# Kernel optimization log

Hardware: AMD Instinct MI355X
Metric: run time of the kernel (lower is better)

The kernel has to match this reference:

```python
import jax, jax.numpy as jnp
import numpy as np

# Dims
B, C, D, H, W = 2, 64, 16, 64, 64
G = 2            # deformable groups (choose_group(64, 2) -> 2)
K = 27           # 3x3x3 kernel points
GC = C // G      # channels per group
AXIS = (0.5, 1.0, 1.0)   # offset_axis_scale (d, h, w)
EPS = 1e-5
# kernel point offsets for k=3, pad=1, dilation=1: {-1,0,1}^3
_KOFF = np.array([(a, b, c) for a in (-1, 0, 1) for b in (-1, 0, 1) for c in (-1, 0, 1)], dtype=np.float32)


def conv3d(x, w, b=None, pad=0):
    y = jax.lax.conv_general_dilated(x, w, (1, 1, 1), [(pad, pad)] * 3,
                                     dimension_numbers=('NCDHW', 'OIDHW', 'NCDHW'))
    if b is not None:
        y = y + b[None, :, None, None, None]
    return y


def proj1x1(x, w, b=None):
    y = jnp.einsum('oc,bcdhw->bodhw', w, x)
    if b is not None:
        y = y + b[None, :, None, None, None]
    return y


def _trilinear_sample(vflat, pd, ph, pw):
    # vflat: [B,G,GC,DHW]; pd/ph/pw: [B,G,DHW] float sampling coords; zeros padding outside
    d0 = jnp.floor(pd); h0 = jnp.floor(ph); w0 = jnp.floor(pw)
    td, th, tw = pd - d0, ph - h0, pw - w0
    d0 = d0.astype(jnp.int32); h0 = h0.astype(jnp.int32); w0 = w0.astype(jnp.int32)
    acc = jnp.zeros_like(vflat)
    for dd in (0, 1):
        for hh in (0, 1):
            for ww in (0, 1):
                di, hi, wi = d0 + dd, h0 + hh, w0 + ww
                valid = ((di >= 0) & (di < D) & (hi >= 0) & (hi < H) & (wi >= 0) & (wi < W)).astype(vflat.dtype)
                idx = (jnp.clip(di, 0, D - 1) * H + jnp.clip(hi, 0, H - 1)) * W + jnp.clip(wi, 0, W - 1)
                g = jnp.take_along_axis(vflat, jnp.broadcast_to(idx[:, :, None, :], vflat.shape), axis=3)
                wgt = ((td if dd else 1.0 - td) * (th if hh else 1.0 - th) * (tw if ww else 1.0 - tw)) * valid
                acc = acc + g * wgt[:, :, None, :]
    return acc


def setup_inputs() -> dict:
    key = jax.random.key(0)
    ks = jax.random.split(key, 8)
    f = jnp.float32
    s = 1.0 / np.sqrt(C)
    return {
        'x': jax.random.normal(ks[0], (B, C, D, H, W), f),
        'gate': jnp.zeros((), f),
        'pre_w': jax.random.normal(ks[1], (C, C, 1, 1, 1), f) * s,
        'post_w': jax.random.normal(ks[2], (C, C, 1, 1, 1), f) * s,
        'in_proj_w': jax.random.normal(ks[3], (C, C), f) * s,
        'in_proj_b': jnp.zeros((C,), f),
        'out_proj_w': jax.random.normal(ks[4], (C, C), f) * s,
        'out_proj_b': jnp.zeros((C,), f),
        'off_w': jax.random.normal(ks[5], (3 * G * K, C, 3, 3, 3), f) * 0.01,
        'off_b': jnp.zeros((3 * G * K,), f),
        'mask_w': jax.random.normal(ks[6], (G * K, C, 3, 3, 3), f) * 0.01,
        'mask_b': jnp.zeros((G * K,), f),
        'in_gamma': jnp.ones((C,), f),
        'in_beta': jnp.zeros((C,), f),
    }


def reference(x, gate, pre_w, post_w, in_proj_w, in_proj_b, out_proj_w, out_proj_b,
              off_w, off_b, mask_w, mask_b, in_gamma, in_beta):
    DHW = D * H * W
    xp = conv3d(x, pre_w)                                      # pre 1x1
    # --- DCNv3_3D: value projection, learned offsets + softmax modulation mask ---
    v = proj1x1(xp, in_proj_w, in_proj_b).reshape(B, G, GC, DHW)
    off = conv3d(xp, off_w, off_b, pad=1).reshape(B, G, K, 3, DHW)   # warmed-up offset_scale = 1.0
    m = jax.nn.softmax(conv3d(xp, mask_w, mask_b, pad=1).reshape(B, G, K, DHW), axis=2)
    dg, hg, wg = jnp.meshgrid(jnp.arange(D, dtype=jnp.float32),
                              jnp.arange(H, dtype=jnp.float32),
                              jnp.arange(W, dtype=jnp.float32), indexing='ij')
    dg, hg, wg = dg.reshape(-1), hg.reshape(-1), wg.reshape(-1)      # [DHW]
    out = jnp.zeros_like(v)
    for k in range(K):   # fixed small loop over 27 kernel points
        pd = dg + _KOFF[k, 0] + off[:, :, k, 0] * AXIS[0]
        ph = hg + _KOFF[k, 1] + off[:, :, k, 1] * AXIS[1]
        pw = wg + _KOFF[k, 2] + off[:, :, k, 2] * AXIS[2]
        out = out + _trilinear_sample(v, pd, ph, pw) * m[:, :, k, :][:, :, None, :]
    y = out.reshape(B, C, D, H, W)
    y = proj1x1(y, out_proj_w, out_proj_b)
    # InstanceNorm3d + GELU
    mu = y.mean(axis=(2, 3, 4), keepdims=True)
    var = y.var(axis=(2, 3, 4), keepdims=True)
    y = (y - mu) * jax.lax.rsqrt(var + EPS)
    y = y * in_gamma[None, :, None, None, None] + in_beta[None, :, None, None, None]
    y = jax.nn.gelu(y)
    y = conv3d(y, post_w)                                      # post 1x1
    return x + jax.nn.sigmoid(gate) * y
```

## Files before the change

### kernel.cpp

```cpp
#include <hip/hip_runtime.h>
#include <hip/hip_bf16.h>

typedef short short8 __attribute__((ext_vector_type(8)));
typedef float f32x4 __attribute__((ext_vector_type(4)));
typedef _Float16 h2 __attribute__((ext_vector_type(2)));
typedef _Float16 half8 __attribute__((ext_vector_type(8)));
typedef __fp16 fp16x2 __attribute__((ext_vector_type(2)));

#if __has_builtin(__builtin_elementwise_fma)
#define FMA2H(a, b, c) __builtin_elementwise_fma((a), (b), (c))
#else
#define FMA2H(a, b, c) ((a) * (b) + (c))
#endif

namespace {
constexpr int Bn = 2, Cn = 64, Dn = 16, Hn = 64, Wn = 64;
constexpr int Gn = 2, Kn = 27, GCn = 32;
constexpr int DHW = Dn * Hn * Wn;
constexpr int OCn = 216;
constexpr int PD = 18, PH = 66, PW = 66;
constexpr float EPS = 1e-5f;

constexpr int PROWS = 12 * 66;
constexpr int PATCH_B = PROWS * 128;

constexpr size_t XPADH_OFF = 0;
constexpr size_t XPADH_B   = (size_t)Bn * PD * PH * PW * Cn * 2;
constexpr size_t WFRAG_OFF = XPADH_OFF + XPADH_B;
constexpr size_t WFRAG_B   = (size_t)54 * 16 * 64 * 16;
constexpr size_t WV_OFF    = WFRAG_OFF + WFRAG_B;
constexpr size_t WV_B      = 64 * 64 * 4;
constexpr size_t CONV_OFF  = WV_OFF + WV_B;
constexpr size_t CONV_B    = (size_t)Bn * OCn * DHW * 2;
constexpr size_t V_OFF     = CONV_OFF + CONV_B;
constexpr size_t V_B       = (size_t)Bn * Gn * DHW * GCn * 2;
constexpr size_t SAMP_OFF  = V_OFF + V_B;
constexpr size_t SAMP_B    = (size_t)Bn * Gn * DHW * GCn * 2;
constexpr size_t STAT_OFF  = SAMP_OFF + SAMP_B;
constexpr size_t WVH_OFF   = STAT_OFF + 4096;
constexpr size_t WOH_OFF   = WVH_OFF + 8192;
constexpr size_t WPH_OFF   = WOH_OFF + 8192;
}

__device__ inline float b2f(short s) {
  union { float f; unsigned u; } x; x.u = ((unsigned)(unsigned short)s) << 16; return x.f;
}
__device__ inline short f2b(float f) {
  __hip_bfloat16 h = __float2bfloat16(f);
  union { __hip_bfloat16 h; short s; } x; x.h = h; return x.s;
}
__device__ inline int iclamp(int v, int lo, int hi) { return v < lo ? lo : (v > hi ? hi : v); }
__device__ inline h2 u2h2(unsigned u) {
  union { unsigned u; h2 h; } x; x.u = u; return x.h;
}
__device__ inline unsigned h2u(h2 h) {
  union { unsigned u; h2 h; } x; x.h = h; return x.u;
}
__device__ inline h2 pkrtz(float a, float b) {
#if __has_builtin(__builtin_amdgcn_cvt_pkrtz)
  union { fp16x2 p; h2 h; } x;
  x.p = __builtin_amdgcn_cvt_pkrtz(a, b);
  return x.h;
#else
  return (h2){(_Float16)a, (_Float16)b};
#endif
}

__global__ __launch_bounds__(256) void zerofill(uint4* __restrict__ p, int n16) {
  int i = blockIdx.x * 256 + threadIdx.x;
  if (i < n16) p[i] = make_uint4(0, 0, 0, 0);
}

__global__ __launch_bounds__(256) void fillpad(const float* __restrict__ x,
                                               __hip_bfloat16* __restrict__ xpadh) {
  int tid = threadIdx.x;
  int w5 = tid & 31, cq = tid >> 5;
  int p = blockIdx.x * 32 + w5;
  int b = blockIdx.y;
  int w = p & 63, h = (p >> 6) & 63, d = p >> 12;
  const float* xb = x + ((size_t)b * 64 + cq * 8) * DHW + p;
  short8 o8;
#pragma unroll
  for (int j = 0; j < 8; ++j) o8[j] = f2b(xb[(size_t)j * DHW]);
  __hip_bfloat16* ob = xpadh + (size_t)b * (PD * PH * PW * 64)
      + ((((size_t)(d + 1) * 66) + (h + 1)) * 66 + (w + 1)) * 64 + cq * 8;
  *(short8*)ob = o8;
}

__global__ __launch_bounds__(256) void fold_weights(
    const float* __restrict__ pre_w, const float* __restrict__ in_proj_w,
    const float* __restrict__ off_w, const float* __restrict__ mask_w,
    short8* __restrict__ Wfrag, float* __restrict__ Wv) {
  int i = blockIdx.x * 256 + threadIdx.x;
  if (i < 64 * 64) {
    int o = i >> 6, c = i & 63;
    float s = 0.f;
    for (int cp = 0; cp < 64; ++cp) s += in_proj_w[o * 64 + cp] * pre_w[cp * 64 + c];
    Wv[i] = s;
    return;
  }
  int t = i - 64 * 64;
  if (t >= 54 * 16 * 64) return;
  int l = t & 63; int rest = t >> 6;
  int mt = rest & 15; int ks = rest >> 4;
  int oc = mt * 16 + (l & 15);
  int tap = ks >> 1;
  int c0 = (ks & 1) * 32 + (l >> 4) * 8;
  float vals[8] = {0.f, 0.f, 0.f, 0.f, 0.f, 0.f, 0.f, 0.f};
  if (oc < OCn) {
    const float* cw = (oc < 162) ? (off_w + (size_t)oc * 64 * 27)
                                 : (mask_w + (size_t)(oc - 162) * 64 * 27);
#pragma unroll 1
    for (int cp = 0; cp < 64; ++cp) {
      float wv = cw[cp * 27 + tap];
      const float* pr = pre_w + cp * 64 + c0;
#pragma unroll
      for (int j = 0; j < 8; ++j) vals[j] += wv * pr[j];
    }
  }
  short8 o8;
#pragma unroll
  for (int j = 0; j < 8; ++j) o8[j] = f2b(vals[j]);
  Wfrag[t] = o8;
}

__global__ __launch_bounds__(256) void packw(
    const float* __restrict__ Wv, const float* __restrict__ Wout,
    const float* __restrict__ Wpost, h2* __restrict__ WvH,
    h2* __restrict__ WoutH, h2* __restrict__ WpostH) {
  int i = blockIdx.x * 256 + threadIdx.x;
  if (i < 2048) WvH[i] = pkrtz(Wv[2 * i], Wv[2 * i + 1]);
  else if (i < 4096) { int j = i - 2048; WoutH[j] = pkrtz(Wout[2 * j], Wout[2 * j + 1]); }
  else if (i < 6144) { int j = i - 4096; WpostH[j] = pkrtz(Wpost[2 * j], Wpost[2 * j + 1]); }
}

__global__ __launch_bounds__(256) void vproj(
    const float* __restrict__ x, const h2* __restrict__ WvH,
    const float* __restrict__ vb, _Float16* __restrict__ v) {
  int p = blockIdx.x * 256 + threadIdx.x;
  int b = blockIdx.y;
  const float* xb = x + (size_t)b * Cn * DHW;
  h2 xh[32];
#pragma unroll
  for (int j = 0; j < 32; ++j)
    xh[j] = pkrtz(xb[(2 * j) * DHW + p], xb[(2 * j + 1) * DHW + p]);
#pragma unroll 1
  for (int g = 0; g < Gn; ++g) {
    _Float16 vo[GCn];
#pragma unroll
    for (int jo = 0; jo < GCn; ++jo) {
      int o = g * GCn + jo;
      h2 a = (h2){(_Float16)0.f, (_Float16)0.f};
#pragma unroll
      for (int j = 0; j < 32; ++j) a = FMA2H(WvH[o * 32 + j], xh[j], a);
      vo[jo] = (_Float16)(vb[o] + (float)a[0] + (float)a[1]);
    }
    half8* dst = (half8*)(v + ((size_t)(b * Gn + g) * DHW + p) * GCn);
#pragma unroll
    for (int q = 0; q < 4; ++q) {
      half8 o8;
#pragma unroll
      for (int j = 0; j < 8; ++j) o8[j] = vo[q * 8 + j];
      dst[q] = o8;
    }
  }
}

__global__ __launch_bounds__(512) void conv_mfma(
    const char* __restrict__ xpadh, const char* __restrict__ wfrag,
    const float* __restrict__ off_b, const float* __restrict__ mask_b,
    __hip_bfloat16* __restrict__ convout) {
  __shared__ char lds[PATCH_B];
  int tid = threadIdx.x;
  int h0 = blockIdx.x * 2, d = blockIdx.y, b = blockIdx.z;

  const char* xb = xpadh + (size_t)b * (PD * PH * PW * 128);
  for (int idx = tid; idx < PROWS * 8; idx += 512) {
    int s = idx >> 3, slot = idx & 7;
    int r12 = s / 66, wx = s - r12 * 66;
    int dp = r12 >> 2, hp = r12 & 3;
    const char* g = xb + ((((size_t)(d + dp)) * 66 + (h0 + hp)) * 66 + wx) * 128 + slot * 16;
    *(uint4*)(lds + s * 128 + ((slot ^ (s & 7)) << 4)) = *(const uint4*)g;
  }
  __syncthreads();

  int wid = tid >> 6, l = tid & 63;
  int wm = wid & 3, wn = wid >> 2;
  int lm = l & 15, lk = l >> 4;
  const char* abase = wfrag + ((size_t)((wm * 4) * 64 + l)) * 16;

  f32x4 acc[4][4];
#pragma unroll
  for (int mt = 0; mt < 4; ++mt)
#pragma unroll
    for (int nt = 0; nt < 4; ++nt) acc[mt][nt] = (f32x4){0.f, 0.f, 0.f, 0.f};

  short8 A0[4], B0[4], A1[4], B1[4], A2[4], B2[4];

#define LOADA(KS, A)                                                          \
  {                                                                           \
    const char* ap_ = abase + (KS) * 16384;                                   \
    _Pragma("unroll")                                                         \
    for (int mt = 0; mt < 4; ++mt) A[mt] = *(const short8*)(ap_ + mt * 1024); \
  }
#define LOADB(KS, B)                                                          \
  {                                                                           \
    int tap_ = (KS) >> 1;                                                     \
    int dd_ = tap_ / 9, rem_ = tap_ - dd_ * 9;                                \
    int dh_ = rem_ / 3, dw_ = rem_ - dh_ * 3;                                 \
    int srow_ = (dd_ * 4 + wn + dh_) * 66 + dw_;                              \
    int uslot_ = 4 * ((KS) & 1) + lk;                                         \
    _Pragma("unroll")                                                         \
    for (int nt = 0; nt < 4; ++nt) {                                          \
      int sr_ = srow_ + nt * 16 + lm;                                         \
      B[nt] = *(const short8*)(lds + sr_ * 128 + ((uslot_ ^ (sr_ & 7)) << 4)); \
    }                                                                         \
  }
#define MFMAS(A, B)                                                           \
  __builtin_amdgcn_s_setprio(1);                                              \
  _Pragma("unroll")                                                           \
  for (int mt = 0; mt < 4; ++mt)                                              \
    _Pragma("unroll")                                                         \
    for (int nt = 0; nt < 4; ++nt)                                            \
      acc[mt][nt] = __builtin_amdgcn_mfma_f32_16x16x32_bf16(A[mt], B[nt], acc[mt][nt], 0, 0, 0); \
  __builtin_amdgcn_s_setprio(0);

  LOADA(0, A0) LOADB(0, B0)
  LOADA(1, A1) LOADB(1, B1)
#pragma unroll 1
  for (int ks = 0; ks < 54; ks += 3) {
    LOADA(ks + 2, A2) LOADB(ks + 2, B2)
    MFMAS(A0, B0)
    if (ks + 3 < 54) { LOADA(ks + 3, A0) LOADB(ks + 3, B0) }
    MFMAS(A1, B1)
    if (ks + 4 < 54) { LOADA(ks + 4, A1) LOADB(ks + 4, B1) }
    MFMAS(A2, B2)
  }
#undef LOADA
#undef LOADB
#undef MFMAS

  int pbase = d * 4096 + (h0 + wn) * 64;
#pragma unroll
  for (int mt = 0; mt < 4; ++mt) {
    int oc0 = wm * 64 + mt * 16 + lk * 4;
#pragma unroll
    for (int r = 0; r < 4; ++r) {
      int oc = oc0 + r;
      if (oc < OCn) {
        float bias = (oc < 162) ? off_b[oc] : mask_b[oc - 162];
        size_t orow = ((size_t)b * OCn + oc) * DHW + pbase;
#pragma unroll
        for (int nt = 0; nt < 4; ++nt)
          convout[orow + nt * 16 + lm] = __float2bfloat16(acc[mt][nt][r] + bias);
      }
    }
  }
}

__global__ __launch_bounds__(256) void dcn_sample(
    const __hip_bfloat16* __restrict__ convout, const _Float16* __restrict__ v,
    _Float16* __restrict__ sampled) {
  __shared__ short offm[108 * 64];
  int tid = threadIdx.x;
  int bg = blockIdx.y;
  int b = bg >> 1, g = bg & 1;
  int p0 = blockIdx.x * 64;

  const __hip_bfloat16* cb = convout + (size_t)b * OCn * DHW;
#pragma unroll 1
  for (int idx = tid; idx < 108 * 8; idx += 256) {
    int row = idx >> 3, col = idx & 7;
    int oc = (row < 81) ? (g * 81 + row) : (162 + g * Kn + (row - 81));
    *(uint4*)(offm + row * 64 + col * 8) = *(const uint4*)(cb + (size_t)oc * DHW + p0 + col * 8);
  }
  __syncthreads();

  int pl = tid >> 2, q = tid & 3;
  int p = p0 + pl;
  int w = p & 63, h = (p >> 6) & 63, d = p >> 12;

  float msum = 0.f;
  h2 acc[4];
#pragma unroll
  for (int j = 0; j < 4; ++j) acc[j] = (h2){(_Float16)0.f, (_Float16)0.f};
  const char* vg = (const char*)v + ((size_t)bg * DHW * GCn + q * 8) * 2;

#pragma unroll 1
  for (int k = 0; k < Kn; ++k) {
    float offd = b2f(offm[(3 * k + 0) * 64 + pl]);
    float offh = b2f(offm[(3 * k + 1) * 64 + pl]);
    float offw = b2f(offm[(3 * k + 2) * 64 + pl]);
    float pd = (float)(d + (k / 9) - 1) + offd * 0.5f;
    float ph = (float)(h + ((k / 3) % 3) - 1) + offh;
    float pw = (float)(w + (k % 3) - 1) + offw;
    float fd = floorf(pd), fh = floorf(ph), fw = floorf(pw);
    float td = pd - fd, th = ph - fh, tw = pw - fw;
    int d0 = (int)fd, h0 = (int)fh, w0 = (int)fw;
    float ek = __expf(b2f(offm[(81 + k) * 64 + pl]));
    msum += ek;

    float wd0 = ((unsigned)d0 < (unsigned)Dn) ? (1.f - td) * ek : 0.f;
    float wd1 = ((unsigned)(d0 + 1) < (unsigned)Dn) ? td * ek : 0.f;
    float wh0 = ((unsigned)h0 < (unsigned)Hn) ? (1.f - th) : 0.f;
    float wh1 = ((unsigned)(h0 + 1) < (unsigned)Hn) ? th : 0.f;
    float ww0 = ((unsigned)w0 < (unsigned)Wn) ? (1.f - tw) : 0.f;
    float ww1 = ((unsigned)(w0 + 1) < (unsigned)Wn) ? tw : 0.f;
    int dr0 = iclamp(d0, 0, Dn - 1) << 18, dr1 = iclamp(d0 + 1, 0, Dn - 1) << 18;
    int hr0 = iclamp(h0, 0, Hn - 1) << 12, hr1 = iclamp(h0 + 1, 0, Hn - 1) << 12;
    int wc0 = iclamp(w0, 0, Wn - 1) << 6,  wc1 = iclamp(w0 + 1, 0, Wn - 1) << 6;
    float wdh00 = wd0 * wh0, wdh01 = wd0 * wh1, wdh10 = wd1 * wh0, wdh11 = wd1 * wh1;

#define CORNER(BOFF, WT)                                                \
    {                                                                   \
      _Float16 wh_ = (_Float16)(WT);                                    \
      h2 w2_ = {wh_, wh_};                                              \
      uint4 u_ = *(const uint4*)(vg + (BOFF));                          \
      acc[0] = FMA2H(u2h2(u_.x), w2_, acc[0]);                          \
      acc[1] = FMA2H(u2h2(u_.y), w2_, acc[1]);                          \
      acc[2] = FMA2H(u2h2(u_.z), w2_, acc[2]);                          \
      acc[3] = FMA2H(u2h2(u_.w), w2_, acc[3]);                          \
    }
    CORNER(dr0 + hr0 + wc0, wdh00 * ww0)
    CORNER(dr0 + hr0 + wc1, wdh00 * ww1)
    CORNER(dr0 + hr1 + wc0, wdh01 * ww0)
    CORNER(dr0 + hr1 + wc1, wdh01 * ww1)
    CORNER(dr1 + hr0 + wc0, wdh10 * ww0)
    CORNER(dr1 + hr0 + wc1, wdh10 * ww1)
    CORNER(dr1 + hr1 + wc0, wdh11 * ww0)
    CORNER(dr1 + hr1 + wc1, wdh11 * ww1)
#undef CORNER
  }

  _Float16 rh = (_Float16)(1.f / msum);
  h2 rs2 = {rh, rh};
  uint4 ov;
  ov.x = h2u(acc[0] * rs2);
  ov.y = h2u(acc[1] * rs2);
  ov.z = h2u(acc[2] * rs2);
  ov.w = h2u(acc[3] * rs2);
  *(uint4*)((char*)sampled + ((size_t)bg * DHW + p) * 64 + q * 16) = ov;
}

__global__ __launch_bounds__(256) void outproj(
    const _Float16* __restrict__ sampled, const h2* __restrict__ WoutH,
    const float* __restrict__ ob, __hip_bfloat16* __restrict__ t) {
  int p = blockIdx.x * 256 + threadIdx.x;
  int b = blockIdx.y;
  h2 sv2[32];
#pragma unroll
  for (int g = 0; g < Gn; ++g) {
    const uint4* src = (const uint4*)(sampled + ((size_t)(b * Gn + g) * DHW + p) * GCn);
#pragma unroll
    for (int q = 0; q < 4; ++q) {
      uint4 uu = src[q];
      sv2[g * 16 + q * 4 + 0] = u2h2(uu.x);
      sv2[g * 16 + q * 4 + 1] = u2h2(uu.y);
      sv2[g * 16 + q * 4 + 2] = u2h2(uu.z);
      sv2[g * 16 + q * 4 + 3] = u2h2(uu.w);
    }
  }
#pragma unroll 1
  for (int o = 0; o < Cn; ++o) {
    h2 a = (h2){(_Float16)0.f, (_Float16)0.f};
#pragma unroll
    for (int j = 0; j < 32; ++j) a = FMA2H(WoutH[o * 32 + j], sv2[j], a);
    float s = ob[o] + (float)a[0] + (float)a[1];
    t[((size_t)b * Cn + o) * DHW + p] = __float2bfloat16(s);
  }
}

__global__ __launch_bounds__(256) void stats_k(const __hip_bfloat16* __restrict__ t,
                                               float* __restrict__ stat) {
  int bc = blockIdx.x;
  const short8* tc = (const short8*)(t + (size_t)bc * DHW);
  float s = 0.f, ss = 0.f;
  for (int i = threadIdx.x; i < DHW / 8; i += 256) {
    short8 s8 = tc[i];
#pragma unroll
    for (int j = 0; j < 8; ++j) { float xv = b2f(s8[j]); s += xv; ss += xv * xv; }
  }
#pragma unroll
  for (int o = 32; o > 0; o >>= 1) { s += __shfl_down(s, o); ss += __shfl_down(ss, o); }
  __shared__ float ls[4], lss[4];
  int wid = threadIdx.x >> 6;
  if ((threadIdx.x & 63) == 0) { ls[wid] = s; lss[wid] = ss; }
  __syncthreads();
  if (threadIdx.x == 0) {
    float S = ls[0] + ls[1] + ls[2] + ls[3];
    float SS = lss[0] + lss[1] + lss[2] + lss[3];
    float mu = S / (float)DHW;
    float var = SS / (float)DHW - mu * mu;
    stat[bc * 2 + 0] = mu;
    stat[bc * 2 + 1] = rsqrtf(var + EPS);
  }
}

__global__ __launch_bounds__(256) void finalk(
    const __hip_bfloat16* __restrict__ t, const float* __restrict__ x,
    const float* __restrict__ stat,
    const float* __restrict__ gamma, const float* __restrict__ beta,
    const h2* __restrict__ WpostH, const float* __restrict__ gate, float* out) {
  int p = blockIdx.x * 256 + threadIdx.x;
  int b = blockIdx.y;
  float sg = 1.f / (1.f + __expf(-gate[0]));
  float nv[Cn];
#pragma unroll
  for (int c = 0; c < Cn; ++c) {
    float mu = stat[(b * Cn + c) * 2 + 0];
    float rstd = stat[(b * Cn + c) * 2 + 1];
    float tv = b2f(((const short*)t)[((size_t)b * Cn + c) * DHW + p]);
    float yv = (tv - mu) * rstd * gamma[c] + beta[c];
    float u = 0.7978845608028654f * (yv + 0.044715f * yv * yv * yv);
    float e = __expf(2.f * u);
    float th = 1.f - 2.f / (e + 1.f);
    nv[c] = 0.5f * yv * (1.f + th);
  }
  h2 nh[32];
#pragma unroll
  for (int j = 0; j < 32; ++j) nh[j] = pkrtz(nv[2 * j], nv[2 * j + 1]);
#pragma unroll 1
  for (int o = 0; o < Cn; ++o) {
    h2 a = (h2){(_Float16)0.f, (_Float16)0.f};
#pragma unroll
    for (int j = 0; j < 32; ++j) a = FMA2H(WpostH[o * 32 + j], nh[j], a);
    float s = (float)a[0] + (float)a[1];
    size_t i = ((size_t)b * Cn + o) * DHW + p;
    out[i] = x[i] + sg * s;
  }
}

extern "C" void kernel_launch(void* const* d_in, const int* in_sizes, int n_in,
                              void* d_out, int out_size, void* d_ws, size_t ws_size,
                              hipStream_t stream) {
  const float* x          = (const float*)d_in[0];
  const float* gate       = (const float*)d_in[1];
  const float* pre_w      = (const float*)d_in[2];
  const float* post_w     = (const float*)d_in[3];
  const float* in_proj_w  = (const float*)d_in[4];
  const float* in_proj_b  = (const float*)d_in[5];
  const float* out_proj_w = (const float*)d_in[6];
  const float* out_proj_b = (const float*)d_in[7];
  const float* off_w      = (const float*)d_in[8];
  const float* off_b      = (const float*)d_in[9];
  const float* mask_w     = (const float*)d_in[10];
  const float* mask_b     = (const float*)d_in[11];
  const float* in_gamma   = (const float*)d_in[12];
  const float* in_beta    = (const float*)d_in[13];

  char* ws = (char*)d_ws;
  __hip_bfloat16* xpadh = (__hip_bfloat16*)(ws + XPADH_OFF);
  short8* Wfrag  = (short8*)(ws + WFRAG_OFF);
  float* Wv      = (float*)(ws + WV_OFF);
  __hip_bfloat16* convout = (__hip_bfloat16*)(ws + CONV_OFF);
  _Float16* v       = (_Float16*)(ws + V_OFF);
  _Float16* sampled = (_Float16*)(ws + SAMP_OFF);
  float* stat    = (float*)(ws + STAT_OFF);
  h2* WvH   = (h2*)(ws + WVH_OFF);
  h2* WoutH = (h2*)(ws + WOH_OFF);
  h2* WpostH = (h2*)(ws + WPH_OFF);
  __hip_bfloat16* t = (__hip_bfloat16*)(ws + XPADH_OFF);
  float* out = (float*)d_out;

  int zf16 = (int)(XPADH_B / 16);
  zerofill<<<(zf16 + 255) / 256, 256, 0, stream>>>((uint4*)xpadh, zf16);
  fillpad<<<dim3(DHW / 32, Bn), 256, 0, stream>>>(x, xpadh);
  int foldN = (64 * 64 + 54 * 16 * 64 + 255) / 256;
  fold_weights<<<foldN, 256, 0, stream>>>(pre_w, in_proj_w, off_w, mask_w, Wfrag, Wv);
  packw<<<24, 256, 0, stream>>>(Wv, out_proj_w, post_w, WvH, WoutH, WpostH);
  vproj<<<dim3(DHW / 256, Bn), 256, 0, stream>>>(x, WvH, in_proj_b, v);
  conv_mfma<<<dim3(32, 16, 2), 512, 0, stream>>>((const char*)xpadh, (const char*)Wfrag,
                                                 off_b, mask_b, convout);
  dcn_sample<<<dim3(DHW / 64, Bn * Gn), 256, 0, stream>>>(convout, v, sampled);
  outproj<<<dim3(DHW / 256, Bn), 256, 0, stream>>>(sampled, WoutH, out_proj_b, t);
  stats_k<<<Bn * Cn, 256, 0, stream>>>(t, stat);
  finalk<<<dim3(DHW / 256, Bn), 256, 0, stream>>>(t, x, stat, in_gamma, in_beta,
                                                  WpostH, gate, out);
}
```

Baseline: 396.1 us.

## Move 1x1 projections to bf16 MFMA GEMMs with LDS staging

Replaces the three per-thread packed-fp16 FMA 1x1 projections (value proj, output proj, post proj) with bf16 MFMA 16x16x32 GEMM kernels that stage activations in swizzled LDS and write output through an LDS transpose buffer. The final kernel is split into a norm+GELU pass writing bf16 channel-last data and a separate MFMA post-projection with the residual add. dcn_sample switches its output to bf16 and remaps block indices so the batch/group blocks for neighbouring positions run together. The aim is to remove the scalar ALU-bound projection loops, at the cost of an extra launch, an extra intermediate round trip through memory, and bf16 rounding instead of fp16.

Result: faster. 338.9 us (-14.4%).

```diff
diff --git a/kernel.cpp b/kernel.cpp
--- a/kernel.cpp
+++ b/kernel.cpp
@@ -4,7 +4,6 @@
 typedef short short8 __attribute__((ext_vector_type(8)));
 typedef float f32x4 __attribute__((ext_vector_type(4)));
 typedef _Float16 h2 __attribute__((ext_vector_type(2)));
-typedef _Float16 half8 __attribute__((ext_vector_type(8)));
 typedef __fp16 fp16x2 __attribute__((ext_vector_type(2)));
 
 #if __has_builtin(__builtin_elementwise_fma)
@@ -37,9 +36,10 @@
 constexpr size_t SAMP_OFF  = V_OFF + V_B;
 constexpr size_t SAMP_B    = (size_t)Bn * Gn * DHW * GCn * 2;
 constexpr size_t STAT_OFF  = SAMP_OFF + SAMP_B;
-constexpr size_t WVH_OFF   = STAT_OFF + 4096;
-constexpr size_t WOH_OFF   = WVH_OFF + 8192;
-constexpr size_t WPH_OFF   = WOH_OFF + 8192;
+constexpr size_t VBH_OFF   = STAT_OFF + 4096;
+constexpr size_t VFRAG_OFF = VBH_OFF + 256;
+constexpr size_t OFRAG_OFF = VFRAG_OFF + 8192;
+constexpr size_t PFRAG_OFF = OFRAG_OFF + 8192;
 }
 
 __device__ inline float b2f(short s) {
@@ -124,44 +124,97 @@
   Wfrag[t] = o8;
 }
 
-__global__ __launch_bounds__(256) void packw(
+__global__ __launch_bounds__(256) void packfrag(
     const float* __restrict__ Wv, const float* __restrict__ Wout,
-    const float* __restrict__ Wpost, h2* __restrict__ WvH,
-    h2* __restrict__ WoutH, h2* __restrict__ WpostH) {
+    const float* __restrict__ Wpost, const float* __restrict__ vb,
+    short8* __restrict__ vfrag, short8* __restrict__ ofrag,
+    short8* __restrict__ pfrag, h2* __restrict__ vbh) {
   int i = blockIdx.x * 256 + threadIdx.x;
-  if (i < 2048) WvH[i] = pkrtz(Wv[2 * i], Wv[2 * i + 1]);
-  else if (i < 4096) { int j = i - 2048; WoutH[j] = pkrtz(Wout[2 * j], Wout[2 * j + 1]); }
-  else if (i < 6144) { int j = i - 4096; WpostH[j] = pkrtz(Wpost[2 * j], Wpost[2 * j + 1]); }
-}
-
-__global__ __launch_bounds__(256) void vproj(
-    const float* __restrict__ x, const h2* __restrict__ WvH,
-    const float* __restrict__ vb, _Float16* __restrict__ v) {
-  int p = blockIdx.x * 256 + threadIdx.x;
-  int b = blockIdx.y;
-  const float* xb = x + (size_t)b * Cn * DHW;
-  h2 xh[32];
-#pragma unroll
-  for (int j = 0; j < 32; ++j)
-    xh[j] = pkrtz(xb[(2 * j) * DHW + p], xb[(2 * j + 1) * DHW + p]);
-#pragma unroll 1
-  for (int g = 0; g < Gn; ++g) {
-    _Float16 vo[GCn];
-#pragma unroll
-    for (int jo = 0; jo < GCn; ++jo) {
-      int o = g * GCn + jo;
-      h2 a = (h2){(_Float16)0.f, (_Float16)0.f};
-#pragma unroll
-      for (int j = 0; j < 32; ++j) a = FMA2H(WvH[o * 32 + j], xh[j], a);
-      vo[jo] = (_Float16)(vb[o] + (float)a[0] + (float)a[1]);
-    }
-    half8* dst = (half8*)(v + ((size_t)(b * Gn + g) * DHW + p) * GCn);
-#pragma unroll
-    for (int q = 0; q < 4; ++q) {
-      half8 o8;
-#pragma unroll
-      for (int j = 0; j < 8; ++j) o8[j] = vo[q * 8 + j];
-      dst[q] = o8;
+  if (i < 32) vbh[i] = pkrtz(vb[2 * i], vb[2 * i + 1]);
+  int which = i >> 9;
+  int t = i & 511;
+  int l = t & 63, mt = (t >> 6) & 3, ks = t >> 8;
+  int m = mt * 16 + (l & 15);
+  int k0 = ks * 32 + (l >> 4) * 8;
+  const float* W = (which == 0) ? Wv : (which == 1) ? Wout : Wpost;
+  short8 o;
+#pragma unroll
+  for (int j = 0; j < 8; ++j) o[j] = f2b(W[m * 64 + k0 + j]);
+  if (which == 0) vfrag[t] = o;
+  else if (which == 1) ofrag[t] = o;
+  else pfrag[t] = o;
+}
+
+#define GEMM_MFMA_BODY(FRAG)                                                  \
+  int wid = tid >> 6, l = tid & 63, lm = l & 15, lk = l >> 4;                 \
+  f32x4 acc[4][4];                                                            \
+  _Pragma("unroll")                                                           \
+  for (int mt = 0; mt < 4; ++mt)                                              \
+    _Pragma("unroll")                                                         \
+    for (int nt = 0; nt < 4; ++nt) acc[mt][nt] = (f32x4){0.f, 0.f, 0.f, 0.f}; \
+  _Pragma("unroll")                                                           \
+  for (int ks = 0; ks < 2; ++ks) {                                            \
+    short8 af[4], bf[4];                                                      \
+    _Pragma("unroll")                                                         \
+    for (int mt = 0; mt < 4; ++mt) af[mt] = FRAG[(ks * 4 + mt) * 64 + l];     \
+    _Pragma("unroll")                                                         \
+    for (int nt = 0; nt < 4; ++nt) {                                          \
+      int sr = wid * 64 + nt * 16 + lm;                                       \
+      int us = ks * 4 + lk;                                                   \
+      bf[nt] = *(const short8*)(stg + sr * 128 + ((us ^ (sr & 7)) << 4));     \
+    }                                                                         \
+    _Pragma("unroll")                                                         \
+    for (int mt = 0; mt < 4; ++mt)                                            \
+      _Pragma("unroll")                                                       \
+      for (int nt = 0; nt < 4; ++nt)                                          \
+        acc[mt][nt] = __builtin_amdgcn_mfma_f32_16x16x32_bf16(af[mt], bf[nt], acc[mt][nt], 0, 0, 0); \
+  }
+
+__global__ __launch_bounds__(256) void vproj_mfma(
+    const char* __restrict__ xpadh, const short8* __restrict__ vfrag,
+    const h2* __restrict__ vbh, _Float16* __restrict__ v) {
+  __shared__ char stg[32768];
+  __shared__ char bnc[256 * 144];
+  int tid = threadIdx.x;
+  int p0 = blockIdx.x * 256, b = blockIdx.y;
+  const char* xb = xpadh + (size_t)b * (PD * PH * PW * 128);
+#pragma unroll
+  for (int it = 0; it < 8; ++it) {
+    int idx = it * 256 + tid;
+    int s = idx >> 3, slot = idx & 7;
+    int p = p0 + s, w = p & 63, h = (p >> 6) & 63, d = p >> 12;
+    const char* g = xb + ((((size_t)(d + 1)) * 66 + (h + 1)) * 66 + (w + 1)) * 128 + slot * 16;
+    *(uint4*)(stg + s * 128 + ((slot ^ (s & 7)) << 4)) = *(const uint4*)g;
+  }
+  __syncthreads();
+  GEMM_MFMA_BODY(vfrag)
+#pragma unroll
+  for (int mt = 0; mt < 4; ++mt)
+#pragma unroll
+    for (int nt = 0; nt < 4; ++nt)
+#pragma unroll
+      for (int r = 0; r < 4; ++r) {
+        int pos = wid * 64 + nt * 16 + lm;
+        int oc = mt * 16 + lk * 4 + r;
+        *(_Float16*)(bnc + pos * 144 + oc * 2) = (_Float16)acc[mt][nt][r];
+      }
+  __syncthreads();
+  {
+    int p = p0 + tid;
+    const unsigned* brow = (const unsigned*)(bnc + tid * 144);
+    char* vb0 = (char*)v + ((size_t)(b * 2 + 0) * DHW + p) * 64;
+    char* vb1 = (char*)v + ((size_t)(b * 2 + 1) * DHW + p) * 64;
+#pragma unroll
+    for (int s = 0; s < 8; ++s) {
+      uint4 ov;
+      unsigned* po = (unsigned*)&ov;
+#pragma unroll
+      for (int j = 0; j < 4; ++j) {
+        h2 hv = u2h2(brow[s * 4 + j]) + vbh[s * 4 + j];
+        po[j] = h2u(hv);
+      }
+      if (s < 4) *(uint4*)(vb0 + s * 16) = ov;
+      else       *(uint4*)(vb1 + (s - 4) * 16) = ov;
     }
   }
 }
@@ -260,12 +313,13 @@
 
 __global__ __launch_bounds__(256) void dcn_sample(
     const __hip_bfloat16* __restrict__ convout, const _Float16* __restrict__ v,
-    _Float16* __restrict__ sampled) {
+    short* __restrict__ sampled) {
   __shared__ short offm[108 * 64];
   int tid = threadIdx.x;
-  int bg = blockIdx.y;
+  int id = blockIdx.x;
+  int bg = (id & 7) >> 1;
+  int p0 = (((id >> 3) << 1) + (id & 1)) * 64;
   int b = bg >> 1, g = bg & 1;
-  int p0 = blockIdx.x * 64;
 
   const __hip_bfloat16* cb = convout + (size_t)b * OCn * DHW;
 #pragma unroll 1
@@ -332,41 +386,57 @@
 #undef CORNER
   }
 
-  _Float16 rh = (_Float16)(1.f / msum);
-  h2 rs2 = {rh, rh};
-  uint4 ov;
-  ov.x = h2u(acc[0] * rs2);
-  ov.y = h2u(acc[1] * rs2);
-  ov.z = h2u(acc[2] * rs2);
-  ov.w = h2u(acc[3] * rs2);
-  *(uint4*)((char*)sampled + ((size_t)bg * DHW + p) * 64 + q * 16) = ov;
-}
-
-__global__ __launch_bounds__(256) void outproj(
-    const _Float16* __restrict__ sampled, const h2* __restrict__ WoutH,
+  float rs = 1.f / msum;
+  short8 o8;
+#pragma unroll
+  for (int j = 0; j < 4; ++j) {
+    o8[2 * j]     = f2b((float)acc[j][0] * rs);
+    o8[2 * j + 1] = f2b((float)acc[j][1] * rs);
+  }
+  *(short8*)((char*)sampled + ((size_t)bg * DHW + p) * 64 + q * 16) = o8;
+}
+
+__global__ __launch_bounds__(256) void outproj_mfma(
+    const short* __restrict__ sampled, const short8* __restrict__ ofrag,
     const float* __restrict__ ob, __hip_bfloat16* __restrict__ t) {
-  int p = blockIdx.x * 256 + threadIdx.x;
-  int b = blockIdx.y;
-  h2 sv2[32];
-#pragma unroll
-  for (int g = 0; g < Gn; ++g) {
-    const uint4* src = (const uint4*)(sampled + ((size_t)(b * Gn + g) * DHW + p) * GCn);
-#pragma unroll
-    for (int q = 0; q < 4; ++q) {
-      uint4 uu = src[q];
-      sv2[g * 16 + q * 4 + 0] = u2h2(uu.x);
-      sv2[g * 16 + q * 4 + 1] = u2h2(uu.y);
-      sv2[g * 16 + q * 4 + 2] = u2h2(uu.z);
-      sv2[g * 16 + q * 4 + 3] = u2h2(uu.w);
-    }
-  }
-#pragma unroll 1
-  for (int o = 0; o < Cn; ++o) {
-    h2 a = (h2){(_Float16)0.f, (_Float16)0.f};
-#pragma unroll
-    for (int j = 0; j < 32; ++j) a = FMA2H(WoutH[o * 32 + j], sv2[j], a);
-    float s = ob[o] + (float)a[0] + (float)a[1];
-    t[((size_t)b * Cn + o) * DHW + p] = __float2bfloat16(s);
+  __shared__ char stg[32768];
+  __shared__ char bnc[256 * 144];
+  int tid = threadIdx.x;
+  int p0 = blockIdx.x * 256, b = blockIdx.y;
+#pragma unroll
+  for (int it = 0; it < 8; ++it) {
+    int idx = it * 256 + tid;
+    int s = idx >> 3, slot = idx & 7;
+    int g = slot >> 2;
+    const char* src = (const char*)sampled + ((size_t)(b * 2 + g) * DHW + p0 + s) * 64 + (slot & 3) * 16;
+    *(uint4*)(stg + s * 128 + ((slot ^ (s & 7)) << 4)) = *(const uint4*)src;
+  }
+  __syncthreads();
+  GEMM_MFMA_BODY(ofrag)
+#pragma unroll
+  for (int mt = 0; mt < 4; ++mt)
+#pragma unroll
+    for (int r = 0; r < 4; ++r) {
+      int oc = mt * 16 + lk * 4 + r;
+      float bias = ob[oc];
+#pragma unroll
+      for (int nt = 0; nt < 4; ++nt) {
+        int pos = wid * 64 + nt * 16 + lm;
+        *(short*)(bnc + pos * 144 + oc * 2) = f2b(acc[mt][nt][r] + bias);
+      }
+    }
+  __syncthreads();
+  {
+    int c = tid & 63, pq = tid >> 6;
+    short* trow = (short*)t + ((size_t)b * 64 + c) * DHW + p0 + pq * 64;
+#pragma unroll
+    for (int s8 = 0; s8 < 8; ++s8) {
+      short8 o8;
+#pragma unroll
+      for (int j = 0; j < 8; ++j)
+        o8[j] = *(const short*)(bnc + (pq * 64 + s8 * 8 + j) * 144 + c * 2);
+      *(short8*)(trow + s8 * 8) = o8;
+    }
   }
 }
 
@@ -396,15 +466,13 @@
   }
 }
 
-__global__ __launch_bounds__(256) void finalk(
-    const __hip_bfloat16* __restrict__ t, const float* __restrict__ x,
-    const float* __restrict__ stat,
+__global__ __launch_bounds__(256) void normgelu(
+    const __hip_bfloat16* __restrict__ t, const float* __restrict__ stat,
     const float* __restrict__ gamma, const float* __restrict__ beta,
-    const h2* __restrict__ WpostH, const float* __restrict__ gate, float* out) {
+    short* __restrict__ nvh) {
   int p = blockIdx.x * 256 + threadIdx.x;
   int b = blockIdx.y;
-  float sg = 1.f / (1.f + __expf(-gate[0]));
-  float nv[Cn];
+  short o[64];
 #pragma unroll
   for (int c = 0; c < Cn; ++c) {
     float mu = stat[(b * Cn + c) * 2 + 0];
@@ -414,19 +482,61 @@
     float u = 0.7978845608028654f * (yv + 0.044715f * yv * yv * yv);
     float e = __expf(2.f * u);
     float th = 1.f - 2.f / (e + 1.f);
-    nv[c] = 0.5f * yv * (1.f + th);
-  }
-  h2 nh[32];
-#pragma unroll
-  for (int j = 0; j < 32; ++j) nh[j] = pkrtz(nv[2 * j], nv[2 * j + 1]);
-#pragma unroll 1
-  for (int o = 0; o < Cn; ++o) {
-    h2 a = (h2){(_Float16)0.f, (_Float16)0.f};
-#pragma unroll
-    for (int j = 0; j < 32; ++j) a = FMA2H(WpostH[o * 32 + j], nh[j], a);
-    float s = (float)a[0] + (float)a[1];
-    size_t i = ((size_t)b * Cn + o) * DHW + p;
-    out[i] = x[i] + sg * s;
+    o[c] = f2b(0.5f * yv * (1.f + th));
+  }
+  short* dst = nvh + ((size_t)b * DHW + p) * 64;
+#pragma unroll
+  for (int s8 = 0; s8 < 8; ++s8) {
+    short8 o8;
+#pragma unroll
+    for (int j = 0; j < 8; ++j) o8[j] = o[s8 * 8 + j];
+    *(short8*)(dst + s8 * 8) = o8;
+  }
+}
+
+__global__ __launch_bounds__(256) void post_mfma(
+    const short* __restrict__ nvh, const short8* __restrict__ pfrag,
+    const float* __restrict__ x, const float* __restrict__ gate,
+    float* __restrict__ out) {
+  __shared__ char stg[32768];
+  __shared__ char bnc[256 * 144];
+  int tid = threadIdx.x;
+  int p0 = blockIdx.x * 256, b = blockIdx.y;
+#pragma unroll
+  for (int it = 0; it < 8; ++it) {
+    int idx = it * 256 + tid;
+    int s = idx >> 3, slot = idx & 7;
+    const char* src = (const char*)nvh + ((size_t)b * DHW + p0 + s) * 128 + slot * 16;
+    *(uint4*)(stg + s * 128 + ((slot ^ (s & 7)) << 4)) = *(const uint4*)src;
+  }
+  __syncthreads();
+  GEMM_MFMA_BODY(pfrag)
+#pragma unroll
+  for (int mt = 0; mt < 4; ++mt)
+#pragma unroll
+    for (int nt = 0; nt < 4; ++nt)
+#pragma unroll
+      for (int r = 0; r < 4; ++r) {
+        int pos = wid * 64 + nt * 16 + lm;
+        int oc = mt * 16 + lk * 4 + r;
+        *(short*)(bnc + pos * 144 + oc * 2) = f2b(acc[mt][nt][r]);
+      }
+  __syncthreads();
+  {
+    float sg = 1.f / (1.f + __expf(-gate[0]));
+    int c = tid & 63, pq = tid >> 6;
+    size_t base = ((size_t)b * 64 + c) * DHW + p0 + pq * 64;
+    const float4* x4 = (const float4*)(x + base);
+    float4* o4 = (float4*)(out + base);
+#pragma unroll
+    for (int qd = 0; qd < 16; ++qd) {
+      float4 xv = x4[qd];
+      float v0 = b2f(*(const short*)(bnc + (pq * 64 + qd * 4 + 0) * 144 + c * 2));
+      float v1 = b2f(*(const short*)(bnc + (pq * 64 + qd * 4 + 1) * 144 + c * 2));
+      float v2 = b2f(*(const short*)(bnc + (pq * 64 + qd * 4 + 2) * 144 + c * 2));
+      float v3 = b2f(*(const short*)(bnc + (pq * 64 + qd * 4 + 3) * 144 + c * 2));
+      o4[qd] = make_float4(xv.x + sg * v0, xv.y + sg * v1, xv.z + sg * v2, xv.w + sg * v3);
+    }
   }
 }
 
@@ -453,12 +563,14 @@
   short8* Wfrag  = (short8*)(ws + WFRAG_OFF);
   float* Wv      = (float*)(ws + WV_OFF);
   __hip_bfloat16* convout = (__hip_bfloat16*)(ws + CONV_OFF);
-  _Float16* v       = (_Float16*)(ws + V_OFF);
-  _Float16* sampled = (_Float16*)(ws + SAMP_OFF);
+  _Float16* v    = (_Float16*)(ws + V_OFF);
+  short* sampled = (short*)(ws + SAMP_OFF);
+  short* nvh     = (short*)(ws + SAMP_OFF);
   float* stat    = (float*)(ws + STAT_OFF);
-  h2* WvH   = (h2*)(ws + WVH_OFF);
-  h2* WoutH = (h2*)(ws + WOH_OFF);
-  h2* WpostH = (h2*)(ws + WPH_OFF);
+  h2* vbh        = (h2*)(ws + VBH_OFF);
+  short8* vfrag  = (short8*)(ws + VFRAG_OFF);
+  short8* ofrag  = (short8*)(ws + OFRAG_OFF);
+  short8* pfrag  = (short8*)(ws + PFRAG_OFF);
   __hip_bfloat16* t = (__hip_bfloat16*)(ws + XPADH_OFF);
   float* out = (float*)d_out;
 
@@ -467,13 +579,14 @@
   fillpad<<<dim3(DHW / 32, Bn), 256, 0, stream>>>(x, xpadh);
   int foldN = (64 * 64 + 54 * 16 * 64 + 255) / 256;
   fold_weights<<<foldN, 256, 0, stream>>>(pre_w, in_proj_w, off_w, mask_w, Wfrag, Wv);
-  packw<<<24, 256, 0, stream>>>(Wv, out_proj_w, post_w, WvH, WoutH, WpostH);
-  vproj<<<dim3(DHW / 256, Bn), 256, 0, stream>>>(x, WvH, in_proj_b, v);
+  packfrag<<<6, 256, 0, stream>>>(Wv, out_proj_w, post_w, in_proj_b,
+                                  vfrag, ofrag, pfrag, vbh);
+  vproj_mfma<<<dim3(DHW / 256, Bn), 256, 0, stream>>>((const char*)xpadh, vfrag, vbh, v);
   conv_mfma<<<dim3(32, 16, 2), 512, 0, stream>>>((const char*)xpadh, (const char*)Wfrag,
                                                  off_b, mask_b, convout);
-  dcn_sample<<<dim3(DHW / 64, Bn * Gn), 256, 0, stream>>>(convout, v, sampled);
-  outproj<<<dim3(DHW / 256, Bn), 256, 0, stream>>>(sampled, WoutH, out_proj_b, t);
+  dcn_sample<<<4096, 256, 0, stream>>>(convout, v, sampled);
+  outproj_mfma<<<dim3(DHW / 256, Bn), 256, 0, stream>>>(sampled, ofrag, out_proj_b, t);
   stats_k<<<Bn * Cn, 256, 0, stream>>>(t, stat);
-  finalk<<<dim3(DHW / 256, Bn), 256, 0, stream>>>(t, x, stat, in_gamma, in_beta,
-                                                  WpostH, gate, out);
-}
+  normgelu<<<dim3(DHW / 256, Bn), 256, 0, stream>>>(t, stat, in_gamma, in_beta, nvh);
+  post_mfma<<<dim3(DHW / 256, Bn), 256, 0, stream>>>(nvh, pfrag, x, gate, out);
+}
```
